# Performance work log

Measured on AMD Instinct MI355X. Metric: run time of the kernel, lower is better.

The kernel has to match this reference:

```python
import jax, jax.numpy as jnp
import numpy as np

D_MODEL = 1024
NUM_HEADS = 16
D_HEAD = D_MODEL // NUM_HEADS
B, T = 2, 2048


def setup_inputs() -> dict:
    key = jax.random.key(0)
    kx, kq, kk, kv, ko = jax.random.split(key, 5)
    # xavier_uniform bound for square (D,D) linear weights
    bound = float(np.sqrt(6.0 / (D_MODEL + D_MODEL)))
    uni = lambda k: jax.random.uniform(k, (D_MODEL, D_MODEL), jnp.float32, -bound, bound)
    return {
        "x": jax.random.normal(kx, (B, T, D_MODEL), jnp.float32),
        "Wq": uni(kq),
        "Wk": uni(kk),
        "Wv": uni(kv),
        "Wo": uni(ko),
    }


def _split_heads(x):
    # (B, T, D) -> (B, H, T, d_head)
    b, t, _ = x.shape
    return x.reshape(b, t, NUM_HEADS, D_HEAD).transpose(0, 2, 1, 3)


def _exclusive_output_mod(Y, V):
    dt = V.dtype
    tiny = jnp.asarray(jnp.finfo(dt).tiny, dt)
    eps = jnp.asarray(jnp.finfo(dt).eps, dt)
    v_sq = jnp.sum(V * V, axis=-1, keepdims=True)
    y_dot_v = jnp.sum(Y * V, axis=-1, keepdims=True)
    scale = jnp.where(v_sq > 0, y_dot_v / jnp.maximum(v_sq, tiny), jnp.zeros_like(y_dot_v))
    Z = Y - scale * V
    residual_norm = jnp.linalg.norm(Z, axis=-1, keepdims=True)
    reference_norm = jnp.maximum(
        jnp.linalg.norm(Y, axis=-1, keepdims=True),
        jnp.linalg.norm(V, axis=-1, keepdims=True),
    )
    cleanup_tol = eps * Z.shape[-1] * reference_norm
    return jnp.where((v_sq > 0) & (residual_norm <= cleanup_tol), jnp.zeros_like(Z), Z)


def reference(x, Wq, Wk, Wv, Wo):
    Q = _split_heads(x @ Wq.T)  # (B,H,T,dh)
    K = _split_heads(x @ Wk.T)
    V = _split_heads(x @ Wv.T)
    sm_scale = 1.0 / np.sqrt(D_HEAD)
    scores = jnp.einsum("bhqd,bhkd->bhqk", Q, K) * sm_scale
    P = jax.nn.softmax(scores, axis=-1)
    Y = jnp.einsum("bhqk,bhkd->bhqd", P, V)
    Z = _exclusive_output_mod(Y, V)
    # merge heads: (B,H,T,dh) -> (B,T,D)
    Zm = Z.transpose(0, 2, 1, 3).reshape(x.shape[0], x.shape[1], D_MODEL)
    return Zm @ Wo.T
```

## Files before the change

kernel.cpp:

```cpp
#include <hip/hip_runtime.h>
#include <math.h>

#define DM   1024
#define TTOK 2048
#define NTOK 4096

typedef __bf16 bf16x8 __attribute__((ext_vector_type(8)));
typedef __bf16 bf16x4 __attribute__((ext_vector_type(4)));
typedef float  f32x4  __attribute__((ext_vector_type(4)));
typedef float  f32x16 __attribute__((ext_vector_type(16)));

#define QSCALE 0.18033688011112042f

#if defined(__has_builtin)
#if __has_builtin(__builtin_amdgcn_exp2f)
#define EXP2F(x) __builtin_amdgcn_exp2f(x)
#endif
#endif
#ifndef EXP2F
#define EXP2F(x) exp2f(x)
#endif

#define GLDS16(g, l) __builtin_amdgcn_global_load_lds( \
    (__attribute__((address_space(1))) void*)(g),      \
    (__attribute__((address_space(3))) void*)(l), 16, 0, 0)

__global__ __launch_bounds__(256)
void cvt_all(const float* __restrict__ x,  const float* __restrict__ Wq,
             const float* __restrict__ Wk, const float* __restrict__ Wv,
             const float* __restrict__ Wo, __bf16* __restrict__ dst) {
    size_t g = ((size_t)blockIdx.x * 256 + threadIdx.x) * 8;
    const float* s;
    size_t off;
    const size_t NX = (size_t)NTOK * DM;
    if (g < NX) { s = x; off = g; }
    else {
        size_t gg = g - NX;
        int w = (int)(gg >> 20);
        off = gg & ((1u << 20) - 1);
        s = (w == 0) ? Wq : (w == 1) ? Wk : (w == 2) ? Wv : Wo;
    }
    float4 a = *(const float4*)(s + off);
    float4 b = *(const float4*)(s + off + 4);
    bf16x8 v;
    v[0] = (__bf16)a.x; v[1] = (__bf16)a.y; v[2] = (__bf16)a.z; v[3] = (__bf16)a.w;
    v[4] = (__bf16)b.x; v[5] = (__bf16)b.y; v[6] = (__bf16)b.z; v[7] = (__bf16)b.w;
    *(bf16x8*)(dst + g) = v;
}

#define LSTR 136
#define DBUF 8192

template<int MODE>
__global__ __launch_bounds__(256)
void gemm_bf16(const __bf16* __restrict__ X,
               const __bf16* __restrict__ W0, const __bf16* __restrict__ W1,
               const __bf16* __restrict__ W2,
               __bf16* __restrict__ Oq, __bf16* __restrict__ Ok,
               __bf16* __restrict__ Ovt, float* __restrict__ Of)
{
    const int z = (MODE == 0) ? blockIdx.z : 3;
    const __bf16 *A, *B;
    int m0, n0;
    if (MODE == 0 && z < 2) {
        A = z ? W1 : W0; B = X;
        m0 = blockIdx.y * 128; n0 = blockIdx.x * 128;
    } else if (MODE == 0) {
        A = X; B = W2;
        m0 = blockIdx.x * 128; n0 = blockIdx.y * 128;
    } else {
        A = X; B = W0;
        m0 = blockIdx.y * 128; n0 = blockIdx.x * 128;
    }

    __shared__ __attribute__((aligned(16))) __bf16 smem[128 * LSTR];

    const int tid  = threadIdx.x;
    const int lane = tid & 63;
    const int wave = tid >> 6;
    const int wm = wave & 1, wn = wave >> 1;
    const int col = lane & 15, quad = lane >> 4;

    const __bf16* Ag = A + (size_t)(m0 + (tid >> 2)) * DM + (tid & 3) * 8;
    const __bf16* Bg = B + (size_t)(n0 + (tid >> 2)) * DM + (tid & 3) * 8;
    __bf16* lA = smem + tid * 8;
    __bf16* lB = smem + 4096 + tid * 8;

    f32x4 acc[4][4];
#pragma unroll
    for (int i = 0; i < 4; ++i)
#pragma unroll
        for (int j = 0; j < 4; ++j)
#pragma unroll
            for (int r = 0; r < 4; ++r) acc[i][j][r] = 0.0f;

    GLDS16(Ag,                   lA);
    GLDS16(Ag + (size_t)64 * DM, lA + 2048);
    GLDS16(Bg,                   lB);
    GLDS16(Bg + (size_t)64 * DM, lB + 2048);
    __syncthreads();

    const int nk = DM / 32;
    for (int t = 0; t < nk; ++t) {
        const int cur = (t & 1) * DBUF;
        const int nxt = DBUF - cur;

        if (t + 1 < nk) {
            const int k1 = (t + 1) * 32;
            GLDS16(Ag + k1,                   lA + nxt);
            GLDS16(Ag + (size_t)64 * DM + k1, lA + nxt + 2048);
            GLDS16(Bg + k1,                   lB + nxt);
            GLDS16(Bg + (size_t)64 * DM + k1, lB + nxt + 2048);
        }

        const __bf16* Asr = smem + cur;
        const __bf16* Bsr = smem + cur + 4096;
        bf16x8 af[4], bfr[4];
#pragma unroll
        for (int i = 0; i < 4; ++i)
            af[i] = *(const bf16x8*)&Asr[(wm * 64 + i * 16 + col) * 32 + quad * 8];
#pragma unroll
        for (int j = 0; j < 4; ++j)
            bfr[j] = *(const bf16x8*)&Bsr[(wn * 64 + j * 16 + col) * 32 + quad * 8];
#pragma unroll
        for (int i = 0; i < 4; ++i)
#pragma unroll
            for (int j = 0; j < 4; ++j)
                acc[i][j] = __builtin_amdgcn_mfma_f32_16x16x32_bf16(af[i], bfr[j], acc[i][j], 0, 0, 0);

        __syncthreads();
    }

    if (MODE == 1) {
#pragma unroll
        for (int i = 0; i < 4; ++i)
#pragma unroll
            for (int j = 0; j < 4; ++j) {
                const int mb = m0 + wm * 64 + i * 16 + quad * 4;
                const int n  = n0 + wn * 64 + j * 16 + col;
#pragma unroll
                for (int r = 0; r < 4; ++r)
                    Of[(size_t)(mb + r) * DM + n] = acc[i][j][r];
            }
        return;
    }

    const float sc = (z == 0) ? QSCALE : 1.0f;
#pragma unroll
    for (int i = 0; i < 4; ++i)
#pragma unroll
        for (int j = 0; j < 4; ++j) {
            const int ml = wm * 64 + i * 16 + quad * 4;
            const int nl = wn * 64 + j * 16 + col;
            bf16x4 pk;
#pragma unroll
            for (int r = 0; r < 4; ++r) pk[r] = (__bf16)(acc[i][j][r] * sc);
            *(bf16x4*)&smem[nl * LSTR + ml] = pk;
        }
    __syncthreads();

#pragma unroll
    for (int it = 0; it < 8; ++it) {
        int c   = tid + 256 * it;
        int row = c >> 4;
        int ch  = (c & 15) * 8;
        bf16x8 v = *(const bf16x8*)&smem[row * LSTR + ch];
        if (z < 2) {
            int t  = n0 + row;
            int b  = t >> 11; t &= 2047;
            int hd = m0 + ch;
            int h  = hd >> 6, d = hd & 63;
            *(bf16x8*)&((z ? Ok : Oq)[(((size_t)(b * 16 + h)) * TTOK + t) * 64 + d]) = v;
        } else {
            int hd = n0 + row;
            int h  = hd >> 6, d = hd & 63;
            int t  = m0 + ch;
            int b  = t >> 11; t &= 2047;
            *(bf16x8*)&Ovt[(((size_t)(b * 16 + h)) * 64 + d) * TTOK + t] = v;
        }
    }
}

__global__ __launch_bounds__(256)
void attn_mfma(const __bf16* __restrict__ Qg, const __bf16* __restrict__ Kg,
               const __bf16* __restrict__ Vtg, __bf16* __restrict__ Zm)
{
    const int bh = blockIdx.y;
    const int q0 = blockIdx.x * 128;
    const size_t base = (size_t)bh * TTOK * 64;

    __shared__ __attribute__((aligned(16))) __bf16 Ks[64 * 72];
    __shared__ __attribute__((aligned(16))) __bf16 Vs[64 * 72];
    __shared__ __attribute__((aligned(16))) __bf16 QPs[128 * 72];

    const int tid  = threadIdx.x;
    const int lane = tid & 63, wave = tid >> 6;
    const int c32  = lane & 31, h32 = lane >> 5;

#pragma unroll
    for (int it = 0; it < 2; ++it) {
        int idx = tid + 256 * it;
        int r = idx >> 2, off = (idx & 3) * 16;
        const __bf16* src = Qg + base + (size_t)(q0 + r) * 64 + off;
        *(bf16x8*)&QPs[r * 72 + off]     = *(const bf16x8*)(src);
        *(bf16x8*)&QPs[r * 72 + off + 8] = *(const bf16x8*)(src + 8);
    }
    __syncthreads();
    bf16x8 qf[4];
#pragma unroll
    for (int st = 0; st < 4; ++st)
        qf[st] = *(const bf16x8*)&QPs[(wave * 32 + c32) * 72 + h32 * 8 + st * 16];

    bf16x8 ones;
#pragma unroll
    for (int i = 0; i < 8; ++i) ones[i] = (__bf16)1.0f;

    f32x16 O[2], lacc;
#pragma unroll
    for (int r = 0; r < 16; ++r) { O[0][r] = 0.0f; O[1][r] = 0.0f; lacc[r] = 0.0f; }

    const int rs = tid >> 2, soff = (tid & 3) * 16;

    bf16x8 kr0 = *(const bf16x8*)(Kg  + base + (size_t)rs * 64 + soff);
    bf16x8 kr1 = *(const bf16x8*)(Kg  + base + (size_t)rs * 64 + soff + 8);
    bf16x8 vr0 = *(const bf16x8*)(Vtg + base + (size_t)rs * TTOK + soff);
    bf16x8 vr1 = *(const bf16x8*)(Vtg + base + (size_t)rs * TTOK + soff + 8);

    const int kb_tgt = (q0 >> 6) + (wave >> 1);
    const int qo     = (wave & 1) * 32 + c32;
    float vq[2][16];

    for (int kb = 0; kb < TTOK / 64; ++kb) {
        __syncthreads();
        *(bf16x8*)&Ks[rs * 72 + soff]     = kr0;
        *(bf16x8*)&Ks[rs * 72 + soff + 8] = kr1;
        *(bf16x8*)&Vs[rs * 72 + soff]     = vr0;
        *(bf16x8*)&Vs[rs * 72 + soff + 8] = vr1;
        __syncthreads();

        {
            int kbn = (kb + 1) & (TTOK / 64 - 1);
            const __bf16* kp = Kg  + base + (size_t)(kbn * 64 + rs) * 64 + soff;
            const __bf16* vp = Vtg + base + (size_t)rs * TTOK + kbn * 64 + soff;
            kr0 = *(const bf16x8*)(kp); kr1 = *(const bf16x8*)(kp + 8);
            vr0 = *(const bf16x8*)(vp); vr1 = *(const bf16x8*)(vp + 8);
        }

        f32x16 s0, s1;
#pragma unroll
        for (int r = 0; r < 16; ++r) { s0[r] = 0.0f; s1[r] = 0.0f; }
        __builtin_amdgcn_s_setprio(1);
#pragma unroll
        for (int st = 0; st < 4; ++st) {
            bf16x8 a0 = *(const bf16x8*)&Ks[(c32)      * 72 + h32 * 8 + st * 16];
            bf16x8 a1 = *(const bf16x8*)&Ks[(32 + c32) * 72 + h32 * 8 + st * 16];
            s0 = __builtin_amdgcn_mfma_f32_32x32x16_bf16(a0, qf[st], s0, 0, 0, 0);
            s1 = __builtin_amdgcn_mfma_f32_32x32x16_bf16(a1, qf[st], s1, 0, 0, 0);
        }
        __builtin_amdgcn_s_setprio(0);

#pragma unroll
        for (int kb2 = 0; kb2 < 2; ++kb2) {
#pragma unroll
            for (int g = 0; g < 4; ++g) {
                float p0 = EXP2F(kb2 ? s1[4 * g + 0] : s0[4 * g + 0]);
                float p1 = EXP2F(kb2 ? s1[4 * g + 1] : s0[4 * g + 1]);
                float p2 = EXP2F(kb2 ? s1[4 * g + 2] : s0[4 * g + 2]);
                float p3 = EXP2F(kb2 ? s1[4 * g + 3] : s0[4 * g + 3]);
                bf16x4 pk;
                pk[0] = (__bf16)p0; pk[1] = (__bf16)p1;
                pk[2] = (__bf16)p2; pk[3] = (__bf16)p3;
                *(bf16x4*)&QPs[(wave * 32 + c32) * 72 + kb2 * 32 + g * 8 + h32 * 4] = pk;
            }
        }

        __builtin_amdgcn_s_setprio(1);
#pragma unroll
        for (int ks = 0; ks < 4; ++ks) {
            bf16x8 pf = *(const bf16x8*)&QPs[(wave * 32 + c32) * 72 + h32 * 8 + ks * 16];
            lacc = __builtin_amdgcn_mfma_f32_32x32x16_bf16(ones, pf, lacc, 0, 0, 0);
            bf16x8 v0 = *(const bf16x8*)&Vs[(c32)      * 72 + h32 * 8 + ks * 16];
            bf16x8 v1 = *(const bf16x8*)&Vs[(32 + c32) * 72 + h32 * 8 + ks * 16];
            O[0] = __builtin_amdgcn_mfma_f32_32x32x16_bf16(v0, pf, O[0], 0, 0, 0);
            O[1] = __builtin_amdgcn_mfma_f32_32x32x16_bf16(v1, pf, O[1], 0, 0, 0);
        }
        __builtin_amdgcn_s_setprio(0);

        if (kb == kb_tgt) {
#pragma unroll
            for (int db = 0; db < 2; ++db)
#pragma unroll
                for (int rg = 0; rg < 16; ++rg) {
                    int d = db * 32 + (rg & 3) + 8 * (rg >> 2) + 4 * h32;
                    vq[db][rg] = (float)Vs[d * 72 + qo];
                }
        }
    }

    const float inv = 1.0f / lacc[0];

    const int b = bh >> 4, h = bh & 15;
    const int q = q0 + wave * 32 + c32;
    float y[2][16];
    float yv = 0.f, v2 = 0.f, yy = 0.f;
#pragma unroll
    for (int db = 0; db < 2; ++db)
#pragma unroll
        for (int rg = 0; rg < 16; ++rg) {
            float yval = O[db][rg] * inv;
            float vval = vq[db][rg];
            y[db][rg] = yval;
            yv += yval * vval; v2 += vval * vval; yy += yval * yval;
        }
    yv += __shfl_xor(yv, 32, 64);
    v2 += __shfl_xor(v2, 32, 64);
    yy += __shfl_xor(yy, 32, 64);
    float scl = (v2 > 0.0f) ? yv / fmaxf(v2, 1.1754943508222875e-38f) : 0.0f;
    float zz = 0.f;
    float zvv[2][16];
#pragma unroll
    for (int db = 0; db < 2; ++db)
#pragma unroll
        for (int rg = 0; rg < 16; ++rg) {
            zvv[db][rg] = y[db][rg] - scl * vq[db][rg];
            zz += zvv[db][rg] * zvv[db][rg];
        }
    zz += __shfl_xor(zz, 32, 64);
    float znorm = sqrtf(zz);
    float refn  = fmaxf(sqrtf(yy), sqrtf(v2));
    bool  wipe  = (v2 > 0.0f) && (znorm <= 1.1920928955078125e-07f * 64.0f * refn);
#pragma unroll
    for (int db = 0; db < 2; ++db)
#pragma unroll
        for (int g = 0; g < 4; ++g) {
            bf16x4 pk;
#pragma unroll
            for (int r = 0; r < 4; ++r)
                pk[r] = (__bf16)(wipe ? 0.0f : zvv[db][4 * g + r]);
            int d = db * 32 + 8 * g + 4 * h32;
            *(bf16x4*)&Zm[((size_t)(b * TTOK + q)) * DM + h * 64 + d] = pk;
        }
}

extern "C" void kernel_launch(void* const* d_in, const int* in_sizes, int n_in,
                              void* d_out, int out_size, void* d_ws, size_t ws_size,
                              hipStream_t stream) {
    const float* x  = (const float*)d_in[0];
    const float* Wq = (const float*)d_in[1];
    const float* Wk = (const float*)d_in[2];
    const float* Wv = (const float*)d_in[3];
    const float* Wo = (const float*)d_in[4];

    const size_t NX = (size_t)NTOK * DM;
    const size_t NW = (size_t)DM * DM;
    __bf16* xb  = (__bf16*)d_ws;
    __bf16* wqb = xb  + NX;
    __bf16* wkb = wqb + NW;
    __bf16* wvb = wkb + NW;
    __bf16* wob = wvb + NW;
    __bf16* Qb  = wob + NW;
    __bf16* Kb  = Qb  + NX;
    __bf16* Vtb = Kb  + NX;
    __bf16* Zmb = Vtb + NX;

    cvt_all<<<(NX + 4 * NW) / 2048, 256, 0, stream>>>(x, Wq, Wk, Wv, Wo, xb);

    gemm_bf16<0><<<dim3(32, 8, 3), 256, 0, stream>>>(
        xb, wqb, wkb, wvb, Qb, Kb, Vtb, nullptr);

    attn_mfma<<<dim3(TTOK / 128, 32), 256, 0, stream>>>(Qb, Kb, Vtb, Zmb);

    gemm_bf16<1><<<dim3(8, 32), 256, 0, stream>>>(
        Zmb, wob, nullptr, nullptr, nullptr, nullptr, nullptr, (float*)d_out);
}
```

Measured before the change: 195.6 us.

## Use fragment-major LDS layouts in GEMM and attention, remap output-GEMM block order

Shared-memory tiles in the GEMM and attention kernels are rearranged into a fragment-major order, so each lane's 16-byte MFMA operand sits contiguously by lane index. This is meant to remove LDS bank conflicts and the padded 72-stride layout. The output projection GEMM also remaps block indices into grouped tiles for better L2 reuse, and the s_setprio hints are dropped. The extra index arithmetic and the changed global load pattern (rows grouped per 16) could affect coalescing.

```diff
diff --git a/kernel.cpp b/kernel.cpp
--- a/kernel.cpp
+++ b/kernel.cpp
@@ -70,7 +70,10 @@
         m0 = blockIdx.x * 128; n0 = blockIdx.y * 128;
     } else {
         A = X; B = W0;
-        m0 = blockIdx.y * 128; n0 = blockIdx.x * 128;
+        int f = blockIdx.x + 8 * blockIdx.y;
+        int c = f & 7, i = f >> 3;
+        m0 = (4 * c + (i & 3)) * 128;
+        n0 = (i >> 2) * 128;
     }
 
     __shared__ __attribute__((aligned(16))) __bf16 smem[128 * LSTR];
@@ -81,8 +84,10 @@
     const int wm = wave & 1, wn = wave >> 1;
     const int col = lane & 15, quad = lane >> 4;
 
-    const __bf16* Ag = A + (size_t)(m0 + (tid >> 2)) * DM + (tid & 3) * 8;
-    const __bf16* Bg = B + (size_t)(n0 + (tid >> 2)) * DM + (tid & 3) * 8;
+    const int arow = ((tid >> 6) << 4) + (tid & 15);
+    const int akc  = (tid >> 4) & 3;
+    const __bf16* Ag = A + (size_t)(m0 + arow) * DM + akc * 8;
+    const __bf16* Bg = B + (size_t)(n0 + arow) * DM + akc * 8;
     __bf16* lA = smem + tid * 8;
     __bf16* lB = smem + 4096 + tid * 8;
 
@@ -118,10 +123,10 @@
         bf16x8 af[4], bfr[4];
 #pragma unroll
         for (int i = 0; i < 4; ++i)
-            af[i] = *(const bf16x8*)&Asr[(wm * 64 + i * 16 + col) * 32 + quad * 8];
+            af[i] = *(const bf16x8*)&Asr[((wm * 4 + i) * 64 + lane) * 8];
 #pragma unroll
         for (int j = 0; j < 4; ++j)
-            bfr[j] = *(const bf16x8*)&Bsr[(wn * 64 + j * 16 + col) * 32 + quad * 8];
+            bfr[j] = *(const bf16x8*)&Bsr[((wn * 4 + j) * 64 + lane) * 8];
 #pragma unroll
         for (int i = 0; i < 4; ++i)
 #pragma unroll
@@ -189,9 +194,9 @@
     const int q0 = blockIdx.x * 128;
     const size_t base = (size_t)bh * TTOK * 64;
 
-    __shared__ __attribute__((aligned(16))) __bf16 Ks[64 * 72];
-    __shared__ __attribute__((aligned(16))) __bf16 Vs[64 * 72];
-    __shared__ __attribute__((aligned(16))) __bf16 QPs[128 * 72];
+    __shared__ __attribute__((aligned(16))) __bf16 Kf[4096];
+    __shared__ __attribute__((aligned(16))) __bf16 Vf[4096];
+    __shared__ __attribute__((aligned(16))) __bf16 QPf[8192];
 
     const int tid  = threadIdx.x;
     const int lane = tid & 63, wave = tid >> 6;
@@ -200,16 +205,17 @@
 #pragma unroll
     for (int it = 0; it < 2; ++it) {
         int idx = tid + 256 * it;
-        int r = idx >> 2, off = (idx & 3) * 16;
-        const __bf16* src = Qg + base + (size_t)(q0 + r) * 64 + off;
-        *(bf16x8*)&QPs[r * 72 + off]     = *(const bf16x8*)(src);
-        *(bf16x8*)&QPs[r * 72 + off + 8] = *(const bf16x8*)(src + 8);
+        int r = idx >> 2, c = idx & 3;
+        const __bf16* src = Qg + base + (size_t)(q0 + r) * 64 + c * 16;
+        __bf16* qr = QPf + (r >> 5) * 2048;
+        *(bf16x8*)&qr[(c * 64 + (r & 31)) * 8]      = *(const bf16x8*)(src);
+        *(bf16x8*)&qr[(c * 64 + 32 + (r & 31)) * 8] = *(const bf16x8*)(src + 8);
     }
     __syncthreads();
     bf16x8 qf[4];
 #pragma unroll
     for (int st = 0; st < 4; ++st)
-        qf[st] = *(const bf16x8*)&QPs[(wave * 32 + c32) * 72 + h32 * 8 + st * 16];
+        qf[st] = *(const bf16x8*)&QPf[wave * 2048 + ((st * 2 + h32) * 32 + c32) * 8];
 
     bf16x8 ones;
 #pragma unroll
@@ -219,7 +225,8 @@
 #pragma unroll
     for (int r = 0; r < 16; ++r) { O[0][r] = 0.0f; O[1][r] = 0.0f; lacc[r] = 0.0f; }
 
-    const int rs = tid >> 2, soff = (tid & 3) * 16;
+    const int rs = tid >> 2, cc = tid & 3;
+    const int soff = cc * 16;
 
     bf16x8 kr0 = *(const bf16x8*)(Kg  + base + (size_t)rs * 64 + soff);
     bf16x8 kr1 = *(const bf16x8*)(Kg  + base + (size_t)rs * 64 + soff + 8);
@@ -228,14 +235,15 @@
 
     const int kb_tgt = (q0 >> 6) + (wave >> 1);
     const int qo     = (wave & 1) * 32 + c32;
+    const int qsb    = ((qo >> 4) * 2 + ((qo >> 3) & 1)) * 512 + (qo & 7);
     float vq[2][16];
 
     for (int kb = 0; kb < TTOK / 64; ++kb) {
         __syncthreads();
-        *(bf16x8*)&Ks[rs * 72 + soff]     = kr0;
-        *(bf16x8*)&Ks[rs * 72 + soff + 8] = kr1;
-        *(bf16x8*)&Vs[rs * 72 + soff]     = vr0;
-        *(bf16x8*)&Vs[rs * 72 + soff + 8] = vr1;
+        *(bf16x8*)&Kf[(cc * 128 + rs) * 8]      = kr0;
+        *(bf16x8*)&Kf[(cc * 128 + 64 + rs) * 8] = kr1;
+        *(bf16x8*)&Vf[(cc * 128 + rs) * 8]      = vr0;
+        *(bf16x8*)&Vf[(cc * 128 + 64 + rs) * 8] = vr1;
         __syncthreads();
 
         {
@@ -249,15 +257,13 @@
         f32x16 s0, s1;
 #pragma unroll
         for (int r = 0; r < 16; ++r) { s0[r] = 0.0f; s1[r] = 0.0f; }
-        __builtin_amdgcn_s_setprio(1);
 #pragma unroll
         for (int st = 0; st < 4; ++st) {
-            bf16x8 a0 = *(const bf16x8*)&Ks[(c32)      * 72 + h32 * 8 + st * 16];
-            bf16x8 a1 = *(const bf16x8*)&Ks[(32 + c32) * 72 + h32 * 8 + st * 16];
+            bf16x8 a0 = *(const bf16x8*)&Kf[((st * 2 + h32) * 64 + c32) * 8];
+            bf16x8 a1 = *(const bf16x8*)&Kf[((st * 2 + h32) * 64 + 32 + c32) * 8];
             s0 = __builtin_amdgcn_mfma_f32_32x32x16_bf16(a0, qf[st], s0, 0, 0, 0);
             s1 = __builtin_amdgcn_mfma_f32_32x32x16_bf16(a1, qf[st], s1, 0, 0, 0);
         }
-        __builtin_amdgcn_s_setprio(0);
 
 #pragma unroll
         for (int kb2 = 0; kb2 < 2; ++kb2) {
@@ -270,21 +276,19 @@
                 bf16x4 pk;
                 pk[0] = (__bf16)p0; pk[1] = (__bf16)p1;
                 pk[2] = (__bf16)p2; pk[3] = (__bf16)p3;
-                *(bf16x4*)&QPs[(wave * 32 + c32) * 72 + kb2 * 32 + g * 8 + h32 * 4] = pk;
+                *(bf16x4*)&QPf[wave * 2048 + ((4 * kb2 + g) * 32 + c32) * 8 + h32 * 4] = pk;
             }
         }
 
-        __builtin_amdgcn_s_setprio(1);
 #pragma unroll
         for (int ks = 0; ks < 4; ++ks) {
-            bf16x8 pf = *(const bf16x8*)&QPs[(wave * 32 + c32) * 72 + h32 * 8 + ks * 16];
+            bf16x8 pf = *(const bf16x8*)&QPf[wave * 2048 + ((ks * 2 + h32) * 32 + c32) * 8];
             lacc = __builtin_amdgcn_mfma_f32_32x32x16_bf16(ones, pf, lacc, 0, 0, 0);
-            bf16x8 v0 = *(const bf16x8*)&Vs[(c32)      * 72 + h32 * 8 + ks * 16];
-            bf16x8 v1 = *(const bf16x8*)&Vs[(32 + c32) * 72 + h32 * 8 + ks * 16];
+            bf16x8 v0 = *(const bf16x8*)&Vf[((ks * 2 + h32) * 64 + c32) * 8];
+            bf16x8 v1 = *(const bf16x8*)&Vf[((ks * 2 + h32) * 64 + 32 + c32) * 8];
             O[0] = __builtin_amdgcn_mfma_f32_32x32x16_bf16(v0, pf, O[0], 0, 0, 0);
             O[1] = __builtin_amdgcn_mfma_f32_32x32x16_bf16(v1, pf, O[1], 0, 0, 0);
         }
-        __builtin_amdgcn_s_setprio(0);
 
         if (kb == kb_tgt) {
 #pragma unroll
@@ -292,7 +296,7 @@
 #pragma unroll
                 for (int rg = 0; rg < 16; ++rg) {
                     int d = db * 32 + (rg & 3) + 8 * (rg >> 2) + 4 * h32;
-                    vq[db][rg] = (float)Vs[d * 72 + qo];
+                    vq[db][rg] = (float)Vf[qsb + d * 8];
                 }
         }
     }
```

Result: slower. 208.9 us (+6.8%).

## Double-buffer K/V tiles in attention, compute row sums in registers, remap output GEMM blocks

Applied to the files above, without the earlier changes.

Double-buffers the attention kernel's K/V shared tiles so each iteration needs one barrier instead of two, with the next tile written to the alternate buffer after compute. The softmax denominator is now accumulated from the exp values in registers and combined with one shuffle, which removes the extra ones-vector MFMA per k-step. Q fragments are loaded straight from global memory, skipping the shared-memory staging and its barrier, and the s_setprio hints are dropped. The output projection GEMM gets a grouped block-index remap to improve L2 reuse. Shared memory use in attention grows, which may lower occupancy.

```diff
diff --git a/kernel.cpp b/kernel.cpp
--- a/kernel.cpp
+++ b/kernel.cpp
@@ -70,7 +70,10 @@
         m0 = blockIdx.x * 128; n0 = blockIdx.y * 128;
     } else {
         A = X; B = W0;
-        m0 = blockIdx.y * 128; n0 = blockIdx.x * 128;
+        int f = blockIdx.x + 8 * blockIdx.y;
+        int c = f & 7, i = f >> 3;
+        m0 = (4 * c + (i & 3)) * 128;
+        n0 = (i >> 2) * 128;
     }
 
     __shared__ __attribute__((aligned(16))) __bf16 smem[128 * LSTR];
@@ -189,35 +192,24 @@
     const int q0 = blockIdx.x * 128;
     const size_t base = (size_t)bh * TTOK * 64;
 
-    __shared__ __attribute__((aligned(16))) __bf16 Ks[64 * 72];
-    __shared__ __attribute__((aligned(16))) __bf16 Vs[64 * 72];
-    __shared__ __attribute__((aligned(16))) __bf16 QPs[128 * 72];
+    __shared__ __attribute__((aligned(16))) __bf16 Ks[2][64 * 72];
+    __shared__ __attribute__((aligned(16))) __bf16 Vs[2][64 * 72];
+    __shared__ __attribute__((aligned(16))) __bf16 Ps[128 * 72];
 
     const int tid  = threadIdx.x;
     const int lane = tid & 63, wave = tid >> 6;
     const int c32  = lane & 31, h32 = lane >> 5;
 
-#pragma unroll
-    for (int it = 0; it < 2; ++it) {
-        int idx = tid + 256 * it;
-        int r = idx >> 2, off = (idx & 3) * 16;
-        const __bf16* src = Qg + base + (size_t)(q0 + r) * 64 + off;
-        *(bf16x8*)&QPs[r * 72 + off]     = *(const bf16x8*)(src);
-        *(bf16x8*)&QPs[r * 72 + off + 8] = *(const bf16x8*)(src + 8);
-    }
-    __syncthreads();
     bf16x8 qf[4];
+    const __bf16* qrow = Qg + base + (size_t)(q0 + wave * 32 + c32) * 64 + h32 * 8;
 #pragma unroll
     for (int st = 0; st < 4; ++st)
-        qf[st] = *(const bf16x8*)&QPs[(wave * 32 + c32) * 72 + h32 * 8 + st * 16];
-
-    bf16x8 ones;
-#pragma unroll
-    for (int i = 0; i < 8; ++i) ones[i] = (__bf16)1.0f;
-
-    f32x16 O[2], lacc;
-#pragma unroll
-    for (int r = 0; r < 16; ++r) { O[0][r] = 0.0f; O[1][r] = 0.0f; lacc[r] = 0.0f; }
+        qf[st] = *(const bf16x8*)(qrow + st * 16);
+
+    f32x16 O[2];
+#pragma unroll
+    for (int r = 0; r < 16; ++r) { O[0][r] = 0.0f; O[1][r] = 0.0f; }
+    float lsum = 0.0f;
 
     const int rs = tid >> 2, soff = (tid & 3) * 16;
 
@@ -225,39 +217,37 @@
     bf16x8 kr1 = *(const bf16x8*)(Kg  + base + (size_t)rs * 64 + soff + 8);
     bf16x8 vr0 = *(const bf16x8*)(Vtg + base + (size_t)rs * TTOK + soff);
     bf16x8 vr1 = *(const bf16x8*)(Vtg + base + (size_t)rs * TTOK + soff + 8);
+    *(bf16x8*)&Ks[0][rs * 72 + soff]     = kr0;
+    *(bf16x8*)&Ks[0][rs * 72 + soff + 8] = kr1;
+    *(bf16x8*)&Vs[0][rs * 72 + soff]     = vr0;
+    *(bf16x8*)&Vs[0][rs * 72 + soff + 8] = vr1;
+    {
+        const __bf16* kp = Kg  + base + (size_t)(64 + rs) * 64 + soff;
+        const __bf16* vp = Vtg + base + (size_t)rs * TTOK + 64 + soff;
+        kr0 = *(const bf16x8*)(kp); kr1 = *(const bf16x8*)(kp + 8);
+        vr0 = *(const bf16x8*)(vp); vr1 = *(const bf16x8*)(vp + 8);
+    }
+    __syncthreads();
 
     const int kb_tgt = (q0 >> 6) + (wave >> 1);
     const int qo     = (wave & 1) * 32 + c32;
     float vq[2][16];
 
     for (int kb = 0; kb < TTOK / 64; ++kb) {
-        __syncthreads();
-        *(bf16x8*)&Ks[rs * 72 + soff]     = kr0;
-        *(bf16x8*)&Ks[rs * 72 + soff + 8] = kr1;
-        *(bf16x8*)&Vs[rs * 72 + soff]     = vr0;
-        *(bf16x8*)&Vs[rs * 72 + soff + 8] = vr1;
-        __syncthreads();
-
-        {
-            int kbn = (kb + 1) & (TTOK / 64 - 1);
-            const __bf16* kp = Kg  + base + (size_t)(kbn * 64 + rs) * 64 + soff;
-            const __bf16* vp = Vtg + base + (size_t)rs * TTOK + kbn * 64 + soff;
-            kr0 = *(const bf16x8*)(kp); kr1 = *(const bf16x8*)(kp + 8);
-            vr0 = *(const bf16x8*)(vp); vr1 = *(const bf16x8*)(vp + 8);
-        }
+        const int cur = kb & 1;
+        const __bf16* Kc = Ks[cur];
+        const __bf16* Vc = Vs[cur];
 
         f32x16 s0, s1;
 #pragma unroll
         for (int r = 0; r < 16; ++r) { s0[r] = 0.0f; s1[r] = 0.0f; }
-        __builtin_amdgcn_s_setprio(1);
 #pragma unroll
         for (int st = 0; st < 4; ++st) {
-            bf16x8 a0 = *(const bf16x8*)&Ks[(c32)      * 72 + h32 * 8 + st * 16];
-            bf16x8 a1 = *(const bf16x8*)&Ks[(32 + c32) * 72 + h32 * 8 + st * 16];
+            bf16x8 a0 = *(const bf16x8*)&Kc[(c32)      * 72 + h32 * 8 + st * 16];
+            bf16x8 a1 = *(const bf16x8*)&Kc[(32 + c32) * 72 + h32 * 8 + st * 16];
             s0 = __builtin_amdgcn_mfma_f32_32x32x16_bf16(a0, qf[st], s0, 0, 0, 0);
             s1 = __builtin_amdgcn_mfma_f32_32x32x16_bf16(a1, qf[st], s1, 0, 0, 0);
         }
-        __builtin_amdgcn_s_setprio(0);
 
 #pragma unroll
         for (int kb2 = 0; kb2 < 2; ++kb2) {
@@ -267,24 +257,22 @@
                 float p1 = EXP2F(kb2 ? s1[4 * g + 1] : s0[4 * g + 1]);
                 float p2 = EXP2F(kb2 ? s1[4 * g + 2] : s0[4 * g + 2]);
                 float p3 = EXP2F(kb2 ? s1[4 * g + 3] : s0[4 * g + 3]);
+                lsum += (p0 + p1) + (p2 + p3);
                 bf16x4 pk;
                 pk[0] = (__bf16)p0; pk[1] = (__bf16)p1;
                 pk[2] = (__bf16)p2; pk[3] = (__bf16)p3;
-                *(bf16x4*)&QPs[(wave * 32 + c32) * 72 + kb2 * 32 + g * 8 + h32 * 4] = pk;
+                *(bf16x4*)&Ps[(wave * 32 + c32) * 72 + kb2 * 32 + g * 8 + h32 * 4] = pk;
             }
         }
 
-        __builtin_amdgcn_s_setprio(1);
 #pragma unroll
         for (int ks = 0; ks < 4; ++ks) {
-            bf16x8 pf = *(const bf16x8*)&QPs[(wave * 32 + c32) * 72 + h32 * 8 + ks * 16];
-            lacc = __builtin_amdgcn_mfma_f32_32x32x16_bf16(ones, pf, lacc, 0, 0, 0);
-            bf16x8 v0 = *(const bf16x8*)&Vs[(c32)      * 72 + h32 * 8 + ks * 16];
-            bf16x8 v1 = *(const bf16x8*)&Vs[(32 + c32) * 72 + h32 * 8 + ks * 16];
+            bf16x8 pf = *(const bf16x8*)&Ps[(wave * 32 + c32) * 72 + h32 * 8 + ks * 16];
+            bf16x8 v0 = *(const bf16x8*)&Vc[(c32)      * 72 + h32 * 8 + ks * 16];
+            bf16x8 v1 = *(const bf16x8*)&Vc[(32 + c32) * 72 + h32 * 8 + ks * 16];
             O[0] = __builtin_amdgcn_mfma_f32_32x32x16_bf16(v0, pf, O[0], 0, 0, 0);
             O[1] = __builtin_amdgcn_mfma_f32_32x32x16_bf16(v1, pf, O[1], 0, 0, 0);
         }
-        __builtin_amdgcn_s_setprio(0);
 
         if (kb == kb_tgt) {
 #pragma unroll
@@ -292,12 +280,30 @@
 #pragma unroll
                 for (int rg = 0; rg < 16; ++rg) {
                     int d = db * 32 + (rg & 3) + 8 * (rg >> 2) + 4 * h32;
-                    vq[db][rg] = (float)Vs[d * 72 + qo];
+                    vq[db][rg] = (float)Vc[d * 72 + qo];
                 }
         }
-    }
-
-    const float inv = 1.0f / lacc[0];
+
+        __bf16* Kn = Ks[cur ^ 1];
+        __bf16* Vn = Vs[cur ^ 1];
+        *(bf16x8*)&Kn[rs * 72 + soff]     = kr0;
+        *(bf16x8*)&Kn[rs * 72 + soff + 8] = kr1;
+        *(bf16x8*)&Vn[rs * 72 + soff]     = vr0;
+        *(bf16x8*)&Vn[rs * 72 + soff + 8] = vr1;
+
+        {
+            int kbn = (kb + 2) & (TTOK / 64 - 1);
+            const __bf16* kp = Kg  + base + (size_t)(kbn * 64 + rs) * 64 + soff;
+            const __bf16* vp = Vtg + base + (size_t)rs * TTOK + kbn * 64 + soff;
+            kr0 = *(const bf16x8*)(kp); kr1 = *(const bf16x8*)(kp + 8);
+            vr0 = *(const bf16x8*)(vp); vr1 = *(const bf16x8*)(vp + 8);
+        }
+
+        __syncthreads();
+    }
+
+    const float ltot = lsum + __shfl_xor(lsum, 32, 64);
+    const float inv  = 1.0f / ltot;
 
     const int b = bh >> 4, h = bh & 15;
     const int q = q0 + wave * 32 + c32;
```

After: 188.1 us. 3.8% less time.
